# Performance work log

Hardware: AMD Instinct MI355X
Metric: run time of the kernel (lower is better)

## Reference

```python
import jax, jax.numpy as jnp
import numpy as np

N = 50000        # total nodes (disjoint batch of graphs)
E = 800000       # total edges
F_IN = 8         # node feature dim
S = 6            # edge feature dim
H = 20           # ECC kernel-network hidden size (hidden_states)
N_OUT = 20       # ECC output channels (n_out=hidden_states)
G = 32           # GCN channels
D1 = 16          # first dense
N_GRAPHS = 512   # graphs in batch


def setup_inputs() -> dict:
    key = jax.random.key(0)
    ks = jax.random.split(key, 24)
    r = lambda k, sh, s: jax.random.normal(k, sh, dtype=jnp.float32) * s
    return {
        "x": r(ks[0], (N, F_IN), 1.0),
        "e": r(ks[1], (E, S), 1.0),
        "edge_index": jax.random.randint(ks[2], (2, E), 0, N, dtype=jnp.int32),
        "seg": jnp.sort(jax.random.randint(ks[3], (N,), 0, N_GRAPHS, dtype=jnp.int32)),
        # ECC kernel network: S -> H -> H -> F_IN*N_OUT
        "ecc_w1": r(ks[4], (S, H), 0.4), "ecc_b1": jnp.zeros((H,), jnp.float32),
        "ecc_w2": r(ks[5], (H, H), 0.2), "ecc_b2": jnp.zeros((H,), jnp.float32),
        "ecc_w3": r(ks[6], (H, F_IN * N_OUT), 0.2), "ecc_b3": jnp.zeros((F_IN * N_OUT,), jnp.float32),
        "ecc_root": r(ks[7], (F_IN, N_OUT), 0.3), "ecc_b": jnp.zeros((N_OUT,), jnp.float32),
        "gcn1_w": r(ks[8], (N_OUT, G), 0.2), "gcn1_b": jnp.zeros((G,), jnp.float32),
        "gcn2_w": r(ks[9], (G, G), 0.2), "gcn2_b": jnp.zeros((G,), jnp.float32),
        "d1_w": r(ks[10], (G, D1), 0.2), "d1_b": jnp.zeros((D1,), jnp.float32),
        "d2_w": r(ks[11], (D1, 1), 0.2), "d2_b": jnp.zeros((1,), jnp.float32),
    }


def reference(x, e, edge_index, seg,
              ecc_w1, ecc_b1, ecc_w2, ecc_b2, ecc_w3, ecc_b3, ecc_root, ecc_b,
              gcn1_w, gcn1_b, gcn2_w, gcn2_b, d1_w, d1_b, d2_w, d2_b):
    row, col = edge_index[0], edge_index[1]  # message col -> row

    # --- ECCConv: per-edge MLP produces an [F_IN, N_OUT] filter per edge ---
    h = jax.nn.relu(e @ ecc_w1 + ecc_b1)
    h = jax.nn.relu(h @ ecc_w2 + ecc_b2)
    w_edge = (h @ ecc_w3 + ecc_b3).reshape(E, F_IN, N_OUT)   # [E, F_in, F_out]
    msg = jnp.einsum('ef,efo->eo', x[col], w_edge)            # per-edge message
    agg = jax.ops.segment_sum(msg, row, num_segments=N)
    x1 = jax.nn.relu(agg + x @ ecc_root + ecc_b)              # root + bias + relu

    # --- GCN normalization from the edge list (A + I, symmetric norm) ---
    deg = jax.ops.segment_sum(jnp.ones((E,), x.dtype), row, num_segments=N) + 1.0
    dinv = jax.lax.rsqrt(deg)
    edge_norm = (dinv[row] * dinv[col])[:, None]
    self_norm = (dinv * dinv)[:, None]

    def gcn(hin, W, b):
        hw = hin @ W
        nmsg = jax.ops.segment_sum(edge_norm * hw[col], row, num_segments=N)
        return jax.nn.relu(nmsg + self_norm * hw + b)

    x2 = gcn(x1, gcn1_w, gcn1_b)
    x3 = gcn(x2, gcn2_w, gcn2_b)

    # --- GlobalSumPool over graph ids, then MLP head ---
    pooled = jax.ops.segment_sum(x3, seg, num_segments=N_GRAPHS)  # [n_graphs, G]
    out = (pooled @ d1_w + d1_b) @ d2_w + d2_b                    # [n_graphs, 1]
    return out
```

## Files before the change

### kernel.cpp

```cpp
#include <hip/hip_runtime.h>

#define S_DIM   6
#define H_DIM   20
#define F_INN   8
#define N_OUTC  20
#define G_DIM   32
#define D1_DIM  16
#define NGRAPH  512
#define CAP     32

typedef short short8 __attribute__((ext_vector_type(8)));
typedef float floatx4 __attribute__((ext_vector_type(4)));

__device__ __forceinline__ unsigned short f2bf(float f) {
    unsigned u = __float_as_uint(f);
    return (unsigned short)((u + 0x8000u) >> 16);
}
__device__ __forceinline__ float bf2f(unsigned short s) {
    return __uint_as_float(((unsigned)s) << 16);
}

__global__ __launch_bounds__(256) void prep_kernel(
    const float* __restrict__ w3, const float* __restrict__ b3,
    unsigned short* __restrict__ B3f)
{
    int idx = blockIdx.x * 256 + threadIdx.x;
    if (idx >= 6144) return;
    int jj   = idx & 7;
    int n    = (idx >> 3) & 15;
    int quad = (idx >> 7) & 3;
    int nt   = (idx >> 9) & 1;
    int s    = idx >> 10;
    int K = 32 * s + quad * 8 + jj;
    int o = n + 16 * nt;
    float v = 0.0f;
    if (o < N_OUTC) {
        if (K < 160)      v = w3[(K >> 3) * 160 + (K & 7) * N_OUTC + o];
        else if (K < 168) v = b3[(K - 160) * N_OUTC + o];
    }
    B3f[idx] = f2bf(v);
}

__global__ __launch_bounds__(256) void loc_kernel(
    const int* __restrict__ ei, int E, int* __restrict__ cnt,
    int* __restrict__ loc)
{
    int i = blockIdx.x * 256 + threadIdx.x;
    if (i >= E) return;
    loc[i] = atomicAdd(&cnt[ei[i]], 1);
}

__global__ __launch_bounds__(256) void scanA_kernel(
    const int* __restrict__ deg, int N, int* __restrict__ bsum)
{
    int i = blockIdx.x * 256 + threadIdx.x;
    int v = (i < N) ? deg[i] : 0;
#pragma unroll
    for (int d = 1; d < 64; d <<= 1) v += __shfl_down(v, d, 64);
    __shared__ int ws[4];
    int wid = threadIdx.x >> 6;
    if ((threadIdx.x & 63) == 0) ws[wid] = v;
    __syncthreads();
    if (threadIdx.x == 0) bsum[blockIdx.x] = ws[0] + ws[1] + ws[2] + ws[3];
}

__global__ __launch_bounds__(256) void scanC_kernel(
    const int* __restrict__ deg, int N, const int* __restrict__ bsum, int nbl,
    int E, int* __restrict__ rowptr, float* __restrict__ dinv)
{
    __shared__ int ws[4];
    __shared__ int sboff;
    int t = threadIdx.x;
    {
        int v = (t < nbl && t < blockIdx.x) ? bsum[t] : 0;
#pragma unroll
        for (int d = 1; d < 64; d <<= 1) v += __shfl_down(v, d, 64);
        int wid = t >> 6;
        if ((t & 63) == 0) ws[wid] = v;
        __syncthreads();
        if (t == 0) sboff = ws[0] + ws[1] + ws[2] + ws[3];
        __syncthreads();
    }

    int i = blockIdx.x * 256 + t;
    int d0 = (i < N) ? deg[i] : 0;
    int v = d0;
#pragma unroll
    for (int d = 1; d < 64; d <<= 1) {
        int u = __shfl_up(v, d, 64);
        if ((t & 63) >= d) v += u;
    }
    __shared__ int ws2[4];
    int wid = t >> 6;
    if ((t & 63) == 63) ws2[wid] = v;
    __syncthreads();
    int woff = 0;
    for (int w = 0; w < wid; ++w) woff += ws2[w];
    if (i < N) {
        rowptr[i] = sboff + woff + v - d0;
        dinv[i] = rsqrtf((float)d0 + 1.0f);
    }
    if (blockIdx.x == 0 && t == 0) rowptr[N] = E;
}

__global__ __launch_bounds__(256) void build_kernel(
    const int* __restrict__ ei, int E, const float* __restrict__ e,
    const int* __restrict__ rowptr, const int* __restrict__ loc,
    int4* __restrict__ e_sorted)
{
    int i = blockIdx.x * 256 + threadIdx.x;
    if (i >= E) return;
    int r = ei[i];
    int c = ei[E + i];
    int p = rowptr[r] + loc[i];

    const float2* ep = (const float2*)&e[(size_t)i * S_DIM];
    float2 e0 = ep[0], e1 = ep[1], e2 = ep[2];

    int4 rec;
    rec.x = c;
    rec.y = (int)f2bf(e0.x) | ((int)f2bf(e0.y) << 16);
    rec.z = (int)f2bf(e1.x) | ((int)f2bf(e1.y) << 16);
    rec.w = (int)f2bf(e2.x) | ((int)f2bf(e2.y) << 16);
    e_sorted[p] = rec;
}

__global__ __launch_bounds__(256) void ecc_mfma_kernel(
    const int4* __restrict__ e_sorted, const float* __restrict__ x,
    const int* __restrict__ rowptr, int N, int E,
    const unsigned short* __restrict__ B3f,
    const float* __restrict__ w1, const float* __restrict__ b1,
    const float* __restrict__ w2, const float* __restrict__ b2,
    const float* __restrict__ root, const float* __restrict__ eb,
    const float* __restrict__ g1w,
    float* __restrict__ agg, int* __restrict__ col_sorted,
    unsigned short* __restrict__ hws1)
{
    __shared__ char smem[20480];
    __shared__ float x1buf[CAP * N_OUTC];
    __shared__ int rbounds[2];
    unsigned short (*h2b)[N_OUTC] = (unsigned short (*)[N_OUTC])smem;
    unsigned short (*xb)[F_INN]   = (unsigned short (*)[F_INN])(smem + 10240);
    float* lmsg = (float*)smem;

    int t = threadIdx.x;
    int j0 = blockIdx.x * 256;
    int jend = min(j0 + 256, E);
    int j = j0 + t;

    if (t < 2) {
        int s = (t == 0) ? j0 : (jend - 1);
        int lo = 0, hi = N - 1;
        while (lo < hi) {
            int m = (lo + hi + 1) >> 1;
            if (rowptr[m] <= s) lo = m; else hi = m - 1;
        }
        rbounds[t] = lo;
    }

    if (j < E) {
        int4 rec = e_sorted[j];
        int c = rec.x;
        col_sorted[j] = c;
        float ef[S_DIM] = {
            bf2f((unsigned short)(rec.y & 0xffff)),
            bf2f((unsigned short)((unsigned)rec.y >> 16)),
            bf2f((unsigned short)(rec.z & 0xffff)),
            bf2f((unsigned short)((unsigned)rec.z >> 16)),
            bf2f((unsigned short)(rec.w & 0xffff)),
            bf2f((unsigned short)((unsigned)rec.w >> 16))
        };

        float h1[H_DIM];
#pragma unroll
        for (int jj = 0; jj < H_DIM; ++jj) {
            float a = b1[jj];
#pragma unroll
            for (int s = 0; s < S_DIM; ++s) a = fmaf(ef[s], w1[s * H_DIM + jj], a);
            h1[jj] = fmaxf(a, 0.0f);
        }

        float h2[H_DIM];
#pragma unroll
        for (int jj = 0; jj < H_DIM; ++jj) {
            float a = b2[jj];
#pragma unroll
            for (int k = 0; k < H_DIM; ++k) a = fmaf(h1[k], w2[k * H_DIM + jj], a);
            h2[jj] = fmaxf(a, 0.0f);
        }

        const float4* xp = (const float4*)&x[(size_t)c * F_INN];
        float4 xa = xp[0], xb4 = xp[1];
        float xf[F_INN] = {xa.x, xa.y, xa.z, xa.w, xb4.x, xb4.y, xb4.z, xb4.w};

#pragma unroll
        for (int o = 0; o < N_OUTC; ++o) h2b[t][o] = f2bf(h2[o]);
#pragma unroll
        for (int f = 0; f < F_INN; ++f) xb[t][f] = f2bf(xf[f]);
    } else {
#pragma unroll
        for (int o = 0; o < N_OUTC; ++o) h2b[t][o] = 0;
#pragma unroll
        for (int f = 0; f < F_INN; ++f) xb[t][f] = 0;
    }
    __syncthreads();

    int lane = t & 63;
    int quad = lane >> 4;
    int n = lane & 15;
    const short8* Bg = (const short8*)B3f;
    short8 Bf[12];
#pragma unroll
    for (int s = 0; s < 6; ++s)
#pragma unroll
        for (int nt = 0; nt < 2; ++nt)
            Bf[s * 2 + nt] = Bg[((s * 2 + nt) * 4 + quad) * 16 + n];

    int w = t >> 6;
    floatx4 acc0s[4], acc1s[4];
#pragma unroll
    for (int T = 0; T < 4; ++T) {
        int base = w * 64 + T * 16;
        int m = base + n;

        const short8 xv8 = *(const short8*)&xb[m][0];
        float xfl[F_INN];
#pragma unroll
        for (int jj = 0; jj < F_INN; ++jj) xfl[jj] = bf2f((unsigned short)xv8[jj]);

        floatx4 acc0 = {0.f, 0.f, 0.f, 0.f};
        floatx4 acc1 = {0.f, 0.f, 0.f, 0.f};
#pragma unroll
        for (int s = 0; s < 6; ++s) {
            short8 A = {0, 0, 0, 0, 0, 0, 0, 0};
            if (s < 5) {
                float h = bf2f(h2b[m][4 * s + quad]);
#pragma unroll
                for (int jj = 0; jj < F_INN; ++jj)
                    A[jj] = (short)f2bf(h * xfl[jj]);
            } else if (quad == 0) {
                A = xv8;
            }
            acc0 = __builtin_amdgcn_mfma_f32_16x16x32_bf16(A, Bf[s * 2 + 0], acc0, 0, 0, 0);
            acc1 = __builtin_amdgcn_mfma_f32_16x16x32_bf16(A, Bf[s * 2 + 1], acc1, 0, 0, 0);
        }
        acc0s[T] = acc0;
        acc1s[T] = acc1;
    }
    __syncthreads();

#pragma unroll
    for (int T = 0; T < 4; ++T) {
        int base = w * 64 + T * 16;
#pragma unroll
        for (int r = 0; r < 4; ++r) {
            int row = base + quad * 4 + r;
            lmsg[row * N_OUTC + n] = acc0s[T][r];
            if (n < 4) lmsg[row * N_OUTC + 16 + n] = acc1s[T][r];
        }
    }
    __syncthreads();

    int r0 = rbounds[0], r1 = rbounds[1];
    int nrows = r1 - r0 + 1;
    int work = nrows * 5;
    for (int ww = t; ww < work; ww += 256) {
        int idx = ww / 5;
        int q = ww - idx * 5;
        int row = r0 + idx;
        int a0 = rowptr[row], a1 = rowptr[row + 1];
        int s0 = max(a0, j0), s1 = min(a1, jend);
        float ac0 = 0.f, ac1 = 0.f, ac2 = 0.f, ac3 = 0.f;
        for (int s = s0; s < s1; ++s) {
            const float4 v = *(const float4*)&lmsg[(s - j0) * N_OUTC + q * 4];
            ac0 += v.x; ac1 += v.y; ac2 += v.z; ac3 += v.w;
        }
        bool owned = (a0 >= j0 && a1 <= jend);
        if (owned && idx < CAP) {
            const float4* xp = (const float4*)&x[(size_t)row * F_INN];
            float4 xa = xp[0], xb4 = xp[1];
            float rx[F_INN] = {xa.x, xa.y, xa.z, xa.w, xb4.x, xb4.y, xb4.z, xb4.w};
            float av[4] = {ac0, ac1, ac2, ac3};
#pragma unroll
            for (int u = 0; u < 4; ++u) {
                int oc = q * 4 + u;
                float a = av[u] + eb[oc];
#pragma unroll
                for (int f = 0; f < F_INN; ++f)
                    a = fmaf(rx[f], root[f * N_OUTC + oc], a);
                x1buf[idx * N_OUTC + oc] = fmaxf(a, 0.0f);
            }
        } else {
            float* dst = &agg[(size_t)row * N_OUTC + q * 4];
            if (owned) {
                *(float4*)dst = make_float4(ac0, ac1, ac2, ac3);
            } else {
                unsafeAtomicAdd(dst + 0, ac0);
                unsafeAtomicAdd(dst + 1, ac1);
                unsafeAtomicAdd(dst + 2, ac2);
                unsafeAtomicAdd(dst + 3, ac3);
            }
        }
    }
    __syncthreads();

    int fast = min(nrows, CAP);
    int work2 = fast * 8;
    for (int ww = t; ww < work2; ww += 256) {
        int idx = ww >> 3;
        int qc = ww & 7;
        int row = r0 + idx;
        int a0 = rowptr[row], a1 = rowptr[row + 1];
        if (!(a0 >= j0 && a1 <= jend)) continue;
        float di = rsqrtf((float)(a1 - a0) + 1.0f);
        float m0 = 0.f, m1 = 0.f, m2 = 0.f, m3 = 0.f;
        const float* xr = &x1buf[idx * N_OUTC];
#pragma unroll
        for (int o = 0; o < N_OUTC; ++o) {
            float xv = xr[o];
            const float4 g = *(const float4*)&g1w[o * G_DIM + qc * 4];
            m0 = fmaf(xv, g.x, m0); m1 = fmaf(xv, g.y, m1);
            m2 = fmaf(xv, g.z, m2); m3 = fmaf(xv, g.w, m3);
        }
        unsigned lo32 = (unsigned)f2bf(m0 * di) | ((unsigned)f2bf(m1 * di) << 16);
        unsigned hi32 = (unsigned)f2bf(m2 * di) | ((unsigned)f2bf(m3 * di) << 16);
        *(uint2*)&hws1[(size_t)row * G_DIM + qc * 4] = make_uint2(lo32, hi32);
    }
}

__global__ __launch_bounds__(256) void cleanup_kernel(
    const float* __restrict__ agg, const float* __restrict__ x,
    const int* __restrict__ rowptr, int N,
    const float* __restrict__ root, const float* __restrict__ eb,
    const float* __restrict__ g1w,
    unsigned short* __restrict__ hws1)
{
    int n = blockIdx.x * 256 + threadIdx.x;
    if (n >= N) return;
    int a0 = rowptr[n], a1 = rowptr[n + 1];
    bool contained = (a1 > a0) ? ((a0 >> 8) == ((a1 - 1) >> 8))
                               : ((a0 & 255) != 0);
    if (contained) {
        int target = (a0 >> 8) << 8;
        int lo = 0, hi = N - 1;
        while (lo < hi) {
            int m = (lo + hi + 1) >> 1;
            if (rowptr[m] <= target) lo = m; else hi = m - 1;
        }
        if (n - lo < CAP) return;
    }

    const float4* xp = (const float4*)&x[(size_t)n * F_INN];
    float4 xa = xp[0], xb = xp[1];
    float xf[F_INN] = {xa.x, xa.y, xa.z, xa.w, xb.x, xb.y, xb.z, xb.w};

    float x1[N_OUTC];
#pragma unroll
    for (int o = 0; o < N_OUTC; ++o) {
        float a = agg[(size_t)n * N_OUTC + o] + eb[o];
#pragma unroll
        for (int f = 0; f < F_INN; ++f) a = fmaf(xf[f], root[f * N_OUTC + o], a);
        x1[o] = fmaxf(a, 0.0f);
    }

    float di = rsqrtf((float)(a1 - a0) + 1.0f);
#pragma unroll
    for (int q = 0; q < 4; ++q) {
        short8 o8;
#pragma unroll
        for (int u = 0; u < 8; ++u) {
            int g = q * 8 + u;
            float a = 0.0f;
#pragma unroll
            for (int o = 0; o < N_OUTC; ++o) a = fmaf(x1[o], g1w[o * G_DIM + g], a);
            o8[u] = (short)f2bf(a * di);
        }
        *(short8*)&hws1[(size_t)n * G_DIM + q * 8] = o8;
    }
}

template<bool DO_MATMUL>
__global__ __launch_bounds__(256) void gcn_gather_kernel(
    const unsigned short* __restrict__ hws, const int* __restrict__ rowptr,
    const int* __restrict__ col_sorted, const float* __restrict__ dinv, int N,
    const float* __restrict__ bias, const float* __restrict__ w2,
    unsigned short* __restrict__ outbuf)
{
    __shared__ float x2s[64][33];
    __shared__ float w2s[G_DIM * G_DIM];

    int t = threadIdx.x;
    int nl = t >> 2;
    int q = t & 3;
    int n = blockIdx.x * 64 + nl;

    if (DO_MATMUL) {
        ((float4*)w2s)[t] = ((const float4*)w2)[t];
    }

    float xo[8];
    float di = 0.0f;
    if (n < N) {
        di = dinv[n];
        int j0 = rowptr[n], j1 = rowptr[n + 1];
        short8 sv = *(const short8*)&hws[(size_t)n * G_DIM + q * 8];
        float s[8];
#pragma unroll
        for (int k = 0; k < 8; ++k) s[k] = bf2f((unsigned short)sv[k]);
#pragma unroll 2
        for (int j = j0; j < j1; ++j) {
            int c = col_sorted[j];
            short8 v = *(const short8*)&hws[(size_t)c * G_DIM + q * 8];
#pragma unroll
            for (int k = 0; k < 8; ++k) s[k] += bf2f((unsigned short)v[k]);
        }
#pragma unroll
        for (int k = 0; k < 8; ++k)
            xo[k] = fmaxf(fmaf(di, s[k], bias[q * 8 + k]), 0.0f);
    } else {
#pragma unroll
        for (int k = 0; k < 8; ++k) xo[k] = 0.0f;
    }

    if (DO_MATMUL) {
#pragma unroll
        for (int k = 0; k < 8; ++k) x2s[nl][q * 8 + k] = xo[k];
        __syncthreads();
        if (n < N) {
            float a[8];
#pragma unroll
            for (int k = 0; k < 8; ++k) a[k] = 0.0f;
#pragma unroll
            for (int g = 0; g < G_DIM; ++g) {
                float xv = x2s[nl][g];
#pragma unroll
                for (int k = 0; k < 8; ++k)
                    a[k] = fmaf(xv, w2s[g * G_DIM + q * 8 + k], a[k]);
            }
            short8 o8;
#pragma unroll
            for (int k = 0; k < 8; ++k) o8[k] = (short)f2bf(a[k] * di);
            *(short8*)&outbuf[(size_t)n * G_DIM + q * 8] = o8;
        }
    } else {
        if (n < N) {
            short8 o8;
#pragma unroll
            for (int k = 0; k < 8; ++k) o8[k] = (short)f2bf(xo[k]);
            *(short8*)&outbuf[(size_t)n * G_DIM + q * 8] = o8;
        }
    }
}

__global__ __launch_bounds__(256) void pool_head_kernel(
    const unsigned short* __restrict__ x3, const int* __restrict__ seg, int N,
    const float* __restrict__ d1w, const float* __restrict__ d1b,
    const float* __restrict__ d2w, const float* __restrict__ d2b,
    float* __restrict__ out)
{
    __shared__ float red[8][G_DIM];
    __shared__ float pvec[G_DIM];
    __shared__ int bounds[2];
    int g = blockIdx.x;
    int t = threadIdx.x;
    if (t < 2) {
        int target = g + t;
        int lo = 0, hi = N;
        while (lo < hi) {
            int m = (lo + hi) >> 1;
            if (seg[m] < target) lo = m + 1; else hi = m;
        }
        bounds[t] = lo;
    }
    __syncthreads();
    int n0 = bounds[0], n1 = bounds[1];
    int ch = t & (G_DIM - 1);
    int slice = t >> 5;
    float a = 0.0f;
    for (int n = n0 + slice; n < n1; n += 8)
        a += bf2f(x3[(size_t)n * G_DIM + ch]);
    red[slice][ch] = a;
    __syncthreads();
    if (slice == 0) {
        float s = red[0][ch];
#pragma unroll
        for (int k = 1; k < 8; ++k) s += red[k][ch];
        pvec[ch] = s;
    }
    __syncthreads();
    if (t < 64) {
        float acc = 0.0f;
        if (t < D1_DIM) {
            float tj = d1b[t];
#pragma unroll
            for (int gg = 0; gg < G_DIM; ++gg)
                tj = fmaf(pvec[gg], d1w[gg * D1_DIM + t], tj);
            acc = tj * d2w[t];
        }
#pragma unroll
        for (int d = 1; d < D1_DIM; d <<= 1) acc += __shfl_down(acc, d, 64);
        if (t == 0) out[g] = acc + d2b[0];
    }
}

extern "C" void kernel_launch(void* const* d_in, const int* in_sizes, int n_in,
                              void* d_out, int out_size, void* d_ws, size_t ws_size,
                              hipStream_t stream)
{
    const float* x    = (const float*)d_in[0];
    const float* e    = (const float*)d_in[1];
    const int*   ei   = (const int*)d_in[2];
    const int*   seg  = (const int*)d_in[3];
    const float* w1   = (const float*)d_in[4];
    const float* b1   = (const float*)d_in[5];
    const float* w2   = (const float*)d_in[6];
    const float* b2   = (const float*)d_in[7];
    const float* w3   = (const float*)d_in[8];
    const float* b3   = (const float*)d_in[9];
    const float* root = (const float*)d_in[10];
    const float* eb   = (const float*)d_in[11];
    const float* g1w  = (const float*)d_in[12];
    const float* g1b  = (const float*)d_in[13];
    const float* g2w  = (const float*)d_in[14];
    const float* g2b  = (const float*)d_in[15];
    const float* d1w  = (const float*)d_in[16];
    const float* d1b  = (const float*)d_in[17];
    const float* d2w  = (const float*)d_in[18];
    const float* d2b  = (const float*)d_in[19];

    const int N = in_sizes[3];
    const int E = in_sizes[1] / S_DIM;
    float* out = (float*)d_out;

    const int nbl = (N + 255) / 256;
    const int ebl = (E + 255) / 256;

    char* ws = (char*)d_ws;
    size_t off = 0;
    auto alloc = [&](size_t elems) -> char* {
        char* p = ws + off;
        off += ((elems * 4 + 15) & ~(size_t)15);
        return p;
    };
    int*   cnt        = (int*)  alloc(N);
    float* agg        = (float*)alloc((size_t)N * N_OUTC);
    size_t zero_bytes = off;
    int*   rowptr     = (int*)  alloc(N + 1);
    int*   bsum       = (int*)  alloc(nbl);
    float* dinv       = (float*)alloc(N);
    int*   loc        = (int*)  alloc(E);
    int*   col_sorted = (int*)  alloc(E);
    unsigned short* B3f = (unsigned short*)alloc(6144 / 2);
    int4*  e_sorted   = (int4*) alloc((size_t)E * 4);
    unsigned short* hws1 = (unsigned short*)alloc((size_t)N * G_DIM / 2);
    unsigned short* hws2 = (unsigned short*)alloc((size_t)N * G_DIM / 2);
    unsigned short* x3   = (unsigned short*)alloc((size_t)N * G_DIM / 2);
    (void)ws_size;

    hipMemsetAsync(d_ws, 0, zero_bytes, stream);

    prep_kernel<<<24, 256, 0, stream>>>(w3, b3, B3f);
    loc_kernel<<<ebl, 256, 0, stream>>>(ei, E, cnt, loc);
    scanA_kernel<<<nbl, 256, 0, stream>>>(cnt, N, bsum);
    scanC_kernel<<<nbl, 256, 0, stream>>>(cnt, N, bsum, nbl, E, rowptr, dinv);
    build_kernel<<<ebl, 256, 0, stream>>>(ei, E, e, rowptr, loc, e_sorted);
    ecc_mfma_kernel<<<ebl, 256, 0, stream>>>(e_sorted, x, rowptr, N, E, B3f,
                                             w1, b1, w2, b2, root, eb, g1w,
                                             agg, col_sorted, hws1);
    cleanup_kernel<<<nbl, 256, 0, stream>>>(agg, x, rowptr, N, root, eb, g1w, hws1);
    gcn_gather_kernel<true><<<(N + 63) / 64, 256, 0, stream>>>(
        hws1, rowptr, col_sorted, dinv, N, g1b, g2w, hws2);
    gcn_gather_kernel<false><<<(N + 63) / 64, 256, 0, stream>>>(
        hws2, rowptr, col_sorted, dinv, N, g2b, nullptr, x3);
    pool_head_kernel<<<NGRAPH, 256, 0, stream>>>(x3, seg, N, d1w, d1b, d2w, d2b, out);
}
```

Baseline: 264.4 us.

## Fuse prep into loc kernel, use packed bf16 converts, unroll GCN gather

Merges the B3 weight-prep kernel into the edge-count kernel to save one launch. Replaces the scalar float-to-bf16 conversions across several kernels with packed two-at-a-time hardware conversions. Unrolls the GCN neighbour gather by four, issuing independent loads for more memory-level parallelism, and shrinks shared memory in the non-matmul gather instantiation. The packed conversion uses round-to-nearest-even with NaN handling, which can differ slightly from the old add-and-shift rounding.

```diff
diff --git a/kernel.cpp b/kernel.cpp
--- a/kernel.cpp
+++ b/kernel.cpp
@@ -1,4 +1,5 @@
 #include <hip/hip_runtime.h>
+#include <hip/hip_bf16.h>
 
 #define S_DIM   6
 #define H_DIM   20
@@ -19,33 +20,34 @@
 __device__ __forceinline__ float bf2f(unsigned short s) {
     return __uint_as_float(((unsigned)s) << 16);
 }
-
-__global__ __launch_bounds__(256) void prep_kernel(
+__device__ __forceinline__ unsigned pk2bf(float a, float b) {
+    union { __hip_bfloat162 b2; unsigned u; } cv;
+    cv.b2 = __float22bfloat162_rn(make_float2(a, b));
+    return cv.u;
+}
+
+__global__ __launch_bounds__(256) void loc_kernel(
+    const int* __restrict__ ei, int E, int* __restrict__ cnt,
+    int* __restrict__ loc,
     const float* __restrict__ w3, const float* __restrict__ b3,
     unsigned short* __restrict__ B3f)
 {
-    int idx = blockIdx.x * 256 + threadIdx.x;
-    if (idx >= 6144) return;
-    int jj   = idx & 7;
-    int n    = (idx >> 3) & 15;
-    int quad = (idx >> 7) & 3;
-    int nt   = (idx >> 9) & 1;
-    int s    = idx >> 10;
-    int K = 32 * s + quad * 8 + jj;
-    int o = n + 16 * nt;
-    float v = 0.0f;
-    if (o < N_OUTC) {
-        if (K < 160)      v = w3[(K >> 3) * 160 + (K & 7) * N_OUTC + o];
-        else if (K < 168) v = b3[(K - 160) * N_OUTC + o];
-    }
-    B3f[idx] = f2bf(v);
-}
-
-__global__ __launch_bounds__(256) void loc_kernel(
-    const int* __restrict__ ei, int E, int* __restrict__ cnt,
-    int* __restrict__ loc)
-{
     int i = blockIdx.x * 256 + threadIdx.x;
+    if (i < 6144) {
+        int jj   = i & 7;
+        int n    = (i >> 3) & 15;
+        int quad = (i >> 7) & 3;
+        int nt   = (i >> 9) & 1;
+        int s    = i >> 10;
+        int K = 32 * s + quad * 8 + jj;
+        int o = n + 16 * nt;
+        float v = 0.0f;
+        if (o < N_OUTC) {
+            if (K < 160)      v = w3[(K >> 3) * 160 + (K & 7) * N_OUTC + o];
+            else if (K < 168) v = b3[(K - 160) * N_OUTC + o];
+        }
+        B3f[i] = f2bf(v);
+    }
     if (i >= E) return;
     loc[i] = atomicAdd(&cnt[ei[i]], 1);
 }
@@ -119,9 +121,9 @@
 
     int4 rec;
     rec.x = c;
-    rec.y = (int)f2bf(e0.x) | ((int)f2bf(e0.y) << 16);
-    rec.z = (int)f2bf(e1.x) | ((int)f2bf(e1.y) << 16);
-    rec.w = (int)f2bf(e2.x) | ((int)f2bf(e2.y) << 16);
+    rec.y = (int)pk2bf(e0.x, e0.y);
+    rec.z = (int)pk2bf(e1.x, e1.y);
+    rec.w = (int)pk2bf(e2.x, e2.y);
     e_sorted[p] = rec;
 }
 
@@ -194,14 +196,16 @@
         float xf[F_INN] = {xa.x, xa.y, xa.z, xa.w, xb4.x, xb4.y, xb4.z, xb4.w};
 
 #pragma unroll
-        for (int o = 0; o < N_OUTC; ++o) h2b[t][o] = f2bf(h2[o]);
-#pragma unroll
-        for (int f = 0; f < F_INN; ++f) xb[t][f] = f2bf(xf[f]);
+        for (int p = 0; p < N_OUTC / 2; ++p)
+            *(unsigned*)&h2b[t][2 * p] = pk2bf(h2[2 * p], h2[2 * p + 1]);
+#pragma unroll
+        for (int p = 0; p < F_INN / 2; ++p)
+            *(unsigned*)&xb[t][2 * p] = pk2bf(xf[2 * p], xf[2 * p + 1]);
     } else {
 #pragma unroll
-        for (int o = 0; o < N_OUTC; ++o) h2b[t][o] = 0;
-#pragma unroll
-        for (int f = 0; f < F_INN; ++f) xb[t][f] = 0;
+        for (int p = 0; p < N_OUTC / 2; ++p) *(unsigned*)&h2b[t][2 * p] = 0u;
+#pragma unroll
+        for (int p = 0; p < F_INN / 2; ++p)  *(unsigned*)&xb[t][2 * p] = 0u;
     }
     __syncthreads();
 
@@ -235,9 +239,11 @@
             short8 A = {0, 0, 0, 0, 0, 0, 0, 0};
             if (s < 5) {
                 float h = bf2f(h2b[m][4 * s + quad]);
-#pragma unroll
-                for (int jj = 0; jj < F_INN; ++jj)
-                    A[jj] = (short)f2bf(h * xfl[jj]);
+                union { short8 s8; unsigned u[4]; } av;
+#pragma unroll
+                for (int p = 0; p < 4; ++p)
+                    av.u[p] = pk2bf(h * xfl[2 * p], h * xfl[2 * p + 1]);
+                A = av.s8;
             } else if (quad == 0) {
                 A = xv8;
             }
@@ -322,8 +328,8 @@
             m0 = fmaf(xv, g.x, m0); m1 = fmaf(xv, g.y, m1);
             m2 = fmaf(xv, g.z, m2); m3 = fmaf(xv, g.w, m3);
         }
-        unsigned lo32 = (unsigned)f2bf(m0 * di) | ((unsigned)f2bf(m1 * di) << 16);
-        unsigned hi32 = (unsigned)f2bf(m2 * di) | ((unsigned)f2bf(m3 * di) << 16);
+        unsigned lo32 = pk2bf(m0 * di, m1 * di);
+        unsigned hi32 = pk2bf(m2 * di, m3 * di);
         *(uint2*)&hws1[(size_t)row * G_DIM + qc * 4] = make_uint2(lo32, hi32);
     }
 }
@@ -366,16 +372,19 @@
     float di = rsqrtf((float)(a1 - a0) + 1.0f);
 #pragma unroll
     for (int q = 0; q < 4; ++q) {
-        short8 o8;
+        float a[8];
 #pragma unroll
         for (int u = 0; u < 8; ++u) {
             int g = q * 8 + u;
-            float a = 0.0f;
-#pragma unroll
-            for (int o = 0; o < N_OUTC; ++o) a = fmaf(x1[o], g1w[o * G_DIM + g], a);
-            o8[u] = (short)f2bf(a * di);
-        }
-        *(short8*)&hws1[(size_t)n * G_DIM + q * 8] = o8;
+            float acc = 0.0f;
+#pragma unroll
+            for (int o = 0; o < N_OUTC; ++o) acc = fmaf(x1[o], g1w[o * G_DIM + g], acc);
+            a[u] = acc * di;
+        }
+        union { short8 s8; unsigned u4[4]; } ov;
+#pragma unroll
+        for (int p = 0; p < 4; ++p) ov.u4[p] = pk2bf(a[2 * p], a[2 * p + 1]);
+        *(short8*)&hws1[(size_t)n * G_DIM + q * 8] = ov.s8;
     }
 }
 
@@ -386,8 +395,8 @@
     const float* __restrict__ bias, const float* __restrict__ w2,
     unsigned short* __restrict__ outbuf)
 {
-    __shared__ float x2s[64][33];
-    __shared__ float w2s[G_DIM * G_DIM];
+    __shared__ float x2s[DO_MATMUL ? 64 * 33 : 1];
+    __shared__ float w2s[DO_MATMUL ? G_DIM * G_DIM : 1];
 
     int t = threadIdx.x;
     int nl = t >> 2;
@@ -396,6 +405,7 @@
 
     if (DO_MATMUL) {
         ((float4*)w2s)[t] = ((const float4*)w2)[t];
+        __syncthreads();
     }
 
     float xo[8];
@@ -407,8 +417,22 @@
         float s[8];
 #pragma unroll
         for (int k = 0; k < 8; ++k) s[k] = bf2f((unsigned short)sv[k]);
-#pragma unroll 2
-        for (int j = j0; j < j1; ++j) {
+        int j = j0;
+        for (; j + 4 <= j1; j += 4) {
+            int c0 = col_sorted[j + 0];
+            int c1 = col_sorted[j + 1];
+            int c2 = col_sorted[j + 2];
+            int c3 = col_sorted[j + 3];
+            short8 v0 = *(const short8*)&hws[(size_t)c0 * G_DIM + q * 8];
+            short8 v1 = *(const short8*)&hws[(size_t)c1 * G_DIM + q * 8];
+            short8 v2 = *(const short8*)&hws[(size_t)c2 * G_DIM + q * 8];
+            short8 v3 = *(const short8*)&hws[(size_t)c3 * G_DIM + q * 8];
+#pragma unroll
+            for (int k = 0; k < 8; ++k)
+                s[k] += (bf2f((unsigned short)v0[k]) + bf2f((unsigned short)v1[k]))
+                      + (bf2f((unsigned short)v2[k]) + bf2f((unsigned short)v3[k]));
+        }
+        for (; j < j1; ++j) {
             int c = col_sorted[j];
             short8 v = *(const short8*)&hws[(size_t)c * G_DIM + q * 8];
 #pragma unroll
@@ -424,7 +448,7 @@
 
     if (DO_MATMUL) {
 #pragma unroll
-        for (int k = 0; k < 8; ++k) x2s[nl][q * 8 + k] = xo[k];
+        for (int k = 0; k < 8; ++k) x2s[nl * 33 + q * 8 + k] = xo[k];
         __syncthreads();
         if (n < N) {
             float a[8];
@@ -432,22 +456,22 @@
             for (int k = 0; k < 8; ++k) a[k] = 0.0f;
 #pragma unroll
             for (int g = 0; g < G_DIM; ++g) {
-                float xv = x2s[nl][g];
+                float xv = x2s[nl * 33 + g];
 #pragma unroll
                 for (int k = 0; k < 8; ++k)
                     a[k] = fmaf(xv, w2s[g * G_DIM + q * 8 + k], a[k]);
             }
-            short8 o8;
-#pragma unroll
-            for (int k = 0; k < 8; ++k) o8[k] = (short)f2bf(a[k] * di);
-            *(short8*)&outbuf[(size_t)n * G_DIM + q * 8] = o8;
+            union { short8 s8; unsigned u4[4]; } ov;
+#pragma unroll
+            for (int p = 0; p < 4; ++p) ov.u4[p] = pk2bf(a[2 * p] * di, a[2 * p + 1] * di);
+            *(short8*)&outbuf[(size_t)n * G_DIM + q * 8] = ov.s8;
         }
     } else {
         if (n < N) {
-            short8 o8;
-#pragma unroll
-            for (int k = 0; k < 8; ++k) o8[k] = (short)f2bf(xo[k]);
-            *(short8*)&outbuf[(size_t)n * G_DIM + q * 8] = o8;
+            union { short8 s8; unsigned u4[4]; } ov;
+#pragma unroll
+            for (int p = 0; p < 4; ++p) ov.u4[p] = pk2bf(xo[2 * p], xo[2 * p + 1]);
+            *(short8*)&outbuf[(size_t)n * G_DIM + q * 8] = ov.s8;
         }
     }
 }
@@ -559,8 +583,7 @@
 
     hipMemsetAsync(d_ws, 0, zero_bytes, stream);
 
-    prep_kernel<<<24, 256, 0, stream>>>(w3, b3, B3f);
-    loc_kernel<<<ebl, 256, 0, stream>>>(ei, E, cnt, loc);
+    loc_kernel<<<ebl, 256, 0, stream>>>(ei, E, cnt, loc, w3, b3, B3f);
     scanA_kernel<<<nbl, 256, 0, stream>>>(cnt, N, bsum);
     scanC_kernel<<<nbl, 256, 0, stream>>>(cnt, N, bsum, nbl, E, rowptr, dinv);
     build_kernel<<<ebl, 256, 0, stream>>>(ei, E, e, rowptr, loc, e_sorted);
```

Result: no change. 262.6 us (-0.7%).
